# Optimization experiments

Hardware: AMD Instinct MI355X
Metric: run time of the kernel (lower is better)

## Reference

```python
import jax, jax.numpy as jnp
import numpy as np
import math

TOP_K = 10  # top-k codes kept by SOHO_Pre_VD for negative sampling
EPS_LN = 1e-5


def layer_norm(x, w, b):
    mu = jnp.mean(x, axis=-1, keepdims=True)
    var = jnp.mean((x - mu) ** 2, axis=-1, keepdims=True)
    return (x - mu) * jax.lax.rsqrt(var + EPS_LN) * w + b


def position_encoding_sine(b, l, d):
    # mask is all-ones [b, l]; identical across batch, compute once and broadcast
    h = w = int(math.sqrt(l))
    ones = jnp.ones((h, w), jnp.float32)
    y_embed = jnp.cumsum(ones, axis=0)
    x_embed = jnp.cumsum(ones, axis=1)
    eps = 1e-6
    two_pi = 2.0 * np.pi
    y_embed = y_embed / (y_embed[-1:, :] + eps) * two_pi
    x_embed = x_embed / (x_embed[:, -1:] + eps) * two_pi
    pf = d // 2
    dim_t = jnp.arange(pf, dtype=jnp.float32)
    dim_t = 10000.0 ** (2.0 * jnp.floor(dim_t / 2.0) / pf)
    px = x_embed[:, :, None] / dim_t  # [h, w, pf]
    py = y_embed[:, :, None] / dim_t
    # interleave sin(even), cos(odd)
    px = jnp.stack([jnp.sin(px[..., 0::2]), jnp.cos(px[..., 1::2])], axis=-1).reshape(h, w, pf)
    py = jnp.stack([jnp.sin(py[..., 0::2]), jnp.cos(py[..., 1::2])], axis=-1).reshape(h, w, pf)
    pos = jnp.concatenate([py, px], axis=-1).reshape(l, d)  # [l, d]
    return jnp.broadcast_to(pos, (b, l, d))


def setup_inputs() -> dict:
    key = jax.random.key(0)
    ks = jax.random.split(key, 10)
    B, L, CIN, D, K = 16, 576, 1024, 768, 8192
    s = 0.02
    return {
        "img": jax.random.normal(ks[0], (B, L, CIN), jnp.float32),
        "mask_indices": jax.random.randint(ks[1], (B, 1), 0, L),
        "lin_w": jax.random.normal(ks[2], (D, CIN), jnp.float32) * s,
        "lin_b": jnp.zeros((D,), jnp.float32),
        "ln1_w": jnp.ones((D,), jnp.float32),
        "ln1_b": jnp.zeros((D,), jnp.float32),
        "embed": jax.random.normal(ks[3], (K, D), jnp.float32),
        "pos_w": jax.random.normal(ks[4], (D, D), jnp.float32) * s,
        "pos_b": jnp.zeros((D,), jnp.float32),
        "gate_w": jax.random.normal(ks[5], (2, 2 * D), jnp.float32) * s,
        "gate_b": jnp.zeros((2,), jnp.float32),
        "gate_ln_w": jnp.ones((2,), jnp.float32),
        "gate_ln_b": jnp.zeros((2,), jnp.float32),
        "out_ln_w": jnp.ones((D,), jnp.float32),
        "out_ln_b": jnp.zeros((D,), jnp.float32),
    }


def reference(img, mask_indices, lin_w, lin_b, ln1_w, ln1_b, embed, pos_w, pos_b,
              gate_w, gate_b, gate_ln_w, gate_ln_b, out_ln_w, out_ln_b):
    b, l, _ = img.shape
    d = lin_w.shape[0]
    # self.linear: Linear -> LayerNorm -> ReLU
    xq = jax.nn.relu(layer_norm(img @ lin_w.T + lin_b, ln1_w, ln1_b))  # [b,l,d]
    x = xq.reshape(b * l, d)
    # SOHO VQ: nearest code by L2, straight-through
    d2 = (x * x).sum(-1, keepdims=True) - 2.0 * (x @ embed.T) + (embed * embed).sum(-1)  # [N,K]
    idx = jnp.argmin(d2, axis=-1)  # [N]
    quant = jnp.take(embed, idx, axis=0)
    quantized = x + jax.lax.stop_gradient(quant - x)
    probs = jax.nn.softmax(-d2, axis=-1)
    topk_values, topk_indices = jax.lax.top_k(probs, TOP_K)  # [N,K'],[N,K']
    # pos_align linear
    quantized = quantized @ pos_w.T + pos_b
    emb_pt = quantized.reshape(b, l, d)
    # gated fusion
    g = jnp.concatenate([emb_pt, xq], axis=-1) @ gate_w.T + gate_b  # [b,l,2]
    g = jax.nn.relu(layer_norm(g, gate_ln_w, gate_ln_b))
    score = jax.nn.softmax(g, axis=-1)
    emb_s, img_s = score[..., 0:1], score[..., 1:2]
    emb_pt = emb_pt * emb_s + xq * img_s
    pos = position_encoding_sine(b, l, d)
    # negative index construction (visual_mask is all ones)
    ind = idx.reshape(b, l).astype(jnp.float32)  # [b,l]
    masked_labels = jnp.take_along_axis(ind, mask_indices, axis=1)  # [b,1]
    masked_neg = (ind == masked_labels).astype(jnp.float32)[..., None]  # [b,l,1]
    samp = jax.random.categorical(jax.random.key(42), jnp.log(topk_values))  # [N]
    neg = jnp.take_along_axis(topk_indices, samp[:, None], axis=1).reshape(b, l, 1).astype(jnp.float32)
    neg_at_mask = jnp.take_along_axis(neg[..., 0], mask_indices, axis=1)[..., None]  # [b,1,1]
    neg_idx = neg_at_mask * masked_neg + ind[..., None] * (1.0 - masked_neg)  # [b,l,1]
    neg_idx = neg_idx.reshape(b * l).astype(jnp.int32)
    # one-hot matmul == embedding gather
    neg_q = jnp.take(embed, neg_idx, axis=0).reshape(b, l, d)
    neg_q = neg_q * emb_s + jax.lax.stop_gradient(xq) * img_s
    out_pos = layer_norm(emb_pt + pos, out_ln_w, out_ln_b)
    out_neg = layer_norm(neg_q + pos, out_ln_w, out_ln_b)
    return (out_pos, out_neg)
```

## Files before the change

### kernel.cpp

```cpp
#include <hip/hip_runtime.h>
#include <stdint.h>

#define M_TOT  9216
#define D_     768
#define CIN_   1024
#define KCODE  8192
#define TOPK   10

typedef unsigned short u16;
typedef __bf16 bf16x8 __attribute__((ext_vector_type(8)));
typedef float f32x4 __attribute__((ext_vector_type(4)));


__device__ inline float block_sum(float v, float* red) {
    int t = threadIdx.x;
    red[t] = v;
    __syncthreads();
    #pragma unroll
    for (int s = 128; s > 0; s >>= 1) {
        if (t < s) red[t] += red[t + s];
        __syncthreads();
    }
    float r = red[0];
    __syncthreads();
    return r;
}

__device__ inline unsigned long long umin64(unsigned long long a, unsigned long long b) {
    return (a < b) ? a : b;
}

__device__ inline u16 f2bf(float f) {
    uint32_t u = __float_as_uint(f);
    uint32_t r = (u + 0x7fffu + ((u >> 16) & 1u)) >> 16;
    return (u16)r;
}
__device__ inline float bf2f(u16 h) {
    return __uint_as_float(((uint32_t)h) << 16);
}

__device__ inline unsigned long long shfl_xor_u64(unsigned long long v, int mask) {
    int lo = (int)(uint32_t)v, hi = (int)(uint32_t)(v >> 32);
    lo = __shfl_xor(lo, mask, 64);
    hi = __shfl_xor(hi, mask, 64);
    return ((unsigned long long)(uint32_t)hi << 32) | (uint32_t)lo;
}

#define GLDS(gp, lp) __builtin_amdgcn_global_load_lds( \
    (const __attribute__((address_space(1))) unsigned int*)(gp), \
    (__attribute__((address_space(3))) unsigned int*)(lp), 16, 0, 0)

__global__ __launch_bounds__(256) void k_gemm1_mfma(
    const u16* __restrict__ Ah, const u16* __restrict__ Am, const u16* __restrict__ Al,
    const u16* __restrict__ Bh, const u16* __restrict__ Bm, const u16* __restrict__ Bl,
    const float* __restrict__ bias, float* __restrict__ C)
{
    __shared__ __align__(16) u16 sm[24576];
    const int t = threadIdx.x;
    const int lane = t & 63, wid = t >> 6;
    const int row0 = blockIdx.y * 128, col0 = blockIdx.x * 128;
    const int r16 = lane & 15, kb = lane >> 4;
    const int wr = wid >> 1, wc = wid & 1;
    const int sc = (lane & 3) * 8;
    const int lrow = lane >> 2;

    f32x4 acc[4][4];
    #pragma unroll
    for (int mf = 0; mf < 4; ++mf)
        #pragma unroll
        for (int nf = 0; nf < 4; ++nf)
            acc[mf][nf] = (f32x4){0.f, 0.f, 0.f, 0.f};

    for (int k0 = 0; k0 < CIN_; k0 += 32) {
        __syncthreads();
        #pragma unroll
        for (int i = 0; i < 12; ++i) {
            int mat = i >> 1;
            int c = (i & 1) ? wid + 4 : wid;
            const u16* mp = (mat == 0) ? Ah : (mat == 1) ? Am : (mat == 2) ? Al
                          : (mat == 3) ? Bh : (mat == 4) ? Bm : Bl;
            int rbase = (mat < 3) ? row0 : col0;
            const u16* g = mp + (size_t)(rbase + c * 16 + lrow) * CIN_ + k0 + sc;
            GLDS(g, sm + mat * 4096 + c * 512);
        }
        __syncthreads();

        bf16x8 bh[4], bm[4], bl[4];
        #pragma unroll
        for (int nf = 0; nf < 4; ++nf) {
            int offb = 12288 + (wc * 64 + nf * 16 + r16) * 32 + kb * 8;
            bh[nf] = *(const bf16x8*)(sm + offb);
            bm[nf] = *(const bf16x8*)(sm + offb + 4096);
            bl[nf] = *(const bf16x8*)(sm + offb + 8192);
        }
        #pragma unroll
        for (int mf = 0; mf < 4; ++mf) {
            int offa = (wr * 64 + mf * 16 + r16) * 32 + kb * 8;
            bf16x8 ah = *(const bf16x8*)(sm + offa);
            bf16x8 am = *(const bf16x8*)(sm + offa + 4096);
            bf16x8 al = *(const bf16x8*)(sm + offa + 8192);
            #pragma unroll
            for (int nf = 0; nf < 4; ++nf) {
                acc[mf][nf] = __builtin_amdgcn_mfma_f32_16x16x32_bf16(ah, bh[nf], acc[mf][nf], 0, 0, 0);
                acc[mf][nf] = __builtin_amdgcn_mfma_f32_16x16x32_bf16(ah, bm[nf], acc[mf][nf], 0, 0, 0);
                acc[mf][nf] = __builtin_amdgcn_mfma_f32_16x16x32_bf16(am, bh[nf], acc[mf][nf], 0, 0, 0);
                acc[mf][nf] = __builtin_amdgcn_mfma_f32_16x16x32_bf16(am, bm[nf], acc[mf][nf], 0, 0, 0);
                acc[mf][nf] = __builtin_amdgcn_mfma_f32_16x16x32_bf16(ah, bl[nf], acc[mf][nf], 0, 0, 0);
                acc[mf][nf] = __builtin_amdgcn_mfma_f32_16x16x32_bf16(al, bh[nf], acc[mf][nf], 0, 0, 0);
            }
        }
    }

    #pragma unroll
    for (int mf = 0; mf < 4; ++mf) {
        #pragma unroll
        for (int q = 0; q < 4; ++q) {
            int m = row0 + wr * 64 + mf * 16 + kb * 4 + q;
            #pragma unroll
            for (int nf = 0; nf < 4; ++nf) {
                int n = col0 + wc * 64 + nf * 16 + r16;
                C[(size_t)m * D_ + n] = acc[mf][nf][q] + bias[n];
            }
        }
    }
}

__global__ __launch_bounds__(256) void k_gemm3_mfma(
    const u16* __restrict__ Eh, const u16* __restrict__ El,
    const u16* __restrict__ Ph, const u16* __restrict__ Pl,
    const int* __restrict__ gather,
    const float* __restrict__ bias, float* __restrict__ C)
{
    __shared__ __align__(16) u16 sm[16384];
    const int t = threadIdx.x;
    const int lane = t & 63, wid = t >> 6;
    const int row0 = blockIdx.y * 128, col0 = blockIdx.x * 128;
    const int r16 = lane & 15, kb = lane >> 4;
    const int wr = wid >> 1, wc = wid & 1;
    const int sc = (lane & 3) * 8;
    const int lrow = lane >> 2;

    int gi0 = gather[row0 + wid * 16 + lrow];
    int gi1 = gather[row0 + (wid + 4) * 16 + lrow];

    f32x4 acc[4][4];
    #pragma unroll
    for (int mf = 0; mf < 4; ++mf)
        #pragma unroll
        for (int nf = 0; nf < 4; ++nf)
            acc[mf][nf] = (f32x4){0.f, 0.f, 0.f, 0.f};

    for (int k0 = 0; k0 < D_; k0 += 32) {
        __syncthreads();
        #pragma unroll
        for (int i = 0; i < 8; ++i) {
            int mat = i >> 1;
            int c = (i & 1) ? wid + 4 : wid;
            int grow = (i & 1) ? gi1 : gi0;
            const u16* g;
            if (mat == 0)      g = Eh + (size_t)grow * D_ + k0 + sc;
            else if (mat == 1) g = El + (size_t)grow * D_ + k0 + sc;
            else if (mat == 2) g = Ph + (size_t)(col0 + c * 16 + lrow) * D_ + k0 + sc;
            else               g = Pl + (size_t)(col0 + c * 16 + lrow) * D_ + k0 + sc;
            GLDS(g, sm + mat * 4096 + c * 512);
        }
        __syncthreads();

        bf16x8 bh[4], bl[4];
        #pragma unroll
        for (int nf = 0; nf < 4; ++nf) {
            int offb = 8192 + (wc * 64 + nf * 16 + r16) * 32 + kb * 8;
            bh[nf] = *(const bf16x8*)(sm + offb);
            bl[nf] = *(const bf16x8*)(sm + offb + 4096);
        }
        #pragma unroll
        for (int mf = 0; mf < 4; ++mf) {
            int offa = (wr * 64 + mf * 16 + r16) * 32 + kb * 8;
            bf16x8 ah = *(const bf16x8*)(sm + offa);
            bf16x8 al = *(const bf16x8*)(sm + offa + 4096);
            #pragma unroll
            for (int nf = 0; nf < 4; ++nf) {
                acc[mf][nf] = __builtin_amdgcn_mfma_f32_16x16x32_bf16(ah, bh[nf], acc[mf][nf], 0, 0, 0);
                acc[mf][nf] = __builtin_amdgcn_mfma_f32_16x16x32_bf16(ah, bl[nf], acc[mf][nf], 0, 0, 0);
                acc[mf][nf] = __builtin_amdgcn_mfma_f32_16x16x32_bf16(al, bh[nf], acc[mf][nf], 0, 0, 0);
            }
        }
    }

    #pragma unroll
    for (int mf = 0; mf < 4; ++mf) {
        #pragma unroll
        for (int q = 0; q < 4; ++q) {
            int m = row0 + wr * 64 + mf * 16 + kb * 4 + q;
            #pragma unroll
            for (int nf = 0; nf < 4; ++nf) {
                int n = col0 + wc * 64 + nf * 16 + r16;
                C[(size_t)m * D_ + n] = acc[mf][nf][q] + bias[n];
            }
        }
    }
}

__global__ __launch_bounds__(256) void k_gemm2_mfma(
    const u16* __restrict__ Xh, const u16* __restrict__ Xl,
    const u16* __restrict__ Eh, const u16* __restrict__ El,
    const float* __restrict__ xsq, const float* __restrict__ esq,
    unsigned long long* __restrict__ amin)
{
    __shared__ __align__(16) u16 sm[32768];
    const int t = threadIdx.x;
    const int lane = t & 63, wid = t >> 6;
    const int row0 = blockIdx.y * 128, col0 = blockIdx.x * 128;
    const int r16 = lane & 15, kb = lane >> 4;
    const int wr = wid >> 1, wc = wid & 1;

    f32x4 acc[4][4];
    #pragma unroll
    for (int mf = 0; mf < 4; ++mf)
        #pragma unroll
        for (int nf = 0; nf < 4; ++nf)
            acc[mf][nf] = (f32x4){0.f, 0.f, 0.f, 0.f};

    const u16* sb = (wid == 0) ? Xh : (wid == 1) ? Xl : (wid == 2) ? Eh : El;
    const int rbase = (wid < 2) ? row0 : col0;
    const u16* srcb = sb + (size_t)(rbase + (lane >> 3)) * D_
                         + ((lane & 7) ^ (lane >> 3)) * 8;
    u16* dstb = sm + wid * 8192 + lane * 8;

    const int swz = (r16 & 7);
    for (int kt = 0; kt < 12; ++kt) {
        __syncthreads();
        #pragma unroll
        for (int c = 0; c < 16; ++c) {
            GLDS(srcb + kt * 64 + c * 8 * D_, dstb + c * 512);
        }
        __syncthreads();
        #pragma unroll
        for (int h = 0; h < 2; ++h) {
            const int slot = ((h * 4 + kb) ^ swz) * 8;
            bf16x8 bh[4], bl[4];
            #pragma unroll
            for (int nf = 0; nf < 4; ++nf) {
                int off = (wc * 64 + nf * 16 + r16) * 64 + slot;
                bh[nf] = *(const bf16x8*)(sm + 16384 + off);
                bl[nf] = *(const bf16x8*)(sm + 24576 + off);
            }
            #pragma unroll
            for (int mf = 0; mf < 4; ++mf) {
                int off = (wr * 64 + mf * 16 + r16) * 64 + slot;
                bf16x8 ah = *(const bf16x8*)(sm + off);
                bf16x8 al = *(const bf16x8*)(sm + 8192 + off);
                #pragma unroll
                for (int nf = 0; nf < 4; ++nf) {
                    acc[mf][nf] = __builtin_amdgcn_mfma_f32_16x16x32_bf16(ah, bh[nf], acc[mf][nf], 0, 0, 0);
                    acc[mf][nf] = __builtin_amdgcn_mfma_f32_16x16x32_bf16(ah, bl[nf], acc[mf][nf], 0, 0, 0);
                    acc[mf][nf] = __builtin_amdgcn_mfma_f32_16x16x32_bf16(al, bh[nf], acc[mf][nf], 0, 0, 0);
                }
            }
        }
    }

    float esqv[4];
    #pragma unroll
    for (int nf = 0; nf < 4; ++nf)
        esqv[nf] = esq[col0 + wc * 64 + nf * 16 + r16];

    #pragma unroll
    for (int mf = 0; mf < 4; ++mf) {
        #pragma unroll
        for (int q = 0; q < 4; ++q) {
            int m = row0 + wr * 64 + mf * 16 + kb * 4 + q;
            float xsv = xsq[m];
            unsigned long long best = ~0ull;
            #pragma unroll
            for (int nf = 0; nf < 4; ++nf) {
                int n = col0 + wc * 64 + nf * 16 + r16;
                float d2 = (xsv - 2.0f * acc[mf][nf][q]) + esqv[nf];
                unsigned long long key =
                    ((unsigned long long)__float_as_uint(d2) << 32) | (unsigned)n;
                best = umin64(best, key);
            }
            #pragma unroll
            for (int msk = 1; msk < 16; msk <<= 1)
                best = umin64(best, shfl_xor_u64(best, msk));
            if (r16 == 0) atomicMin(&amin[m], best);
        }
    }
}

__global__ __launch_bounds__(256) void k_split3(const float* __restrict__ in,
    u16* __restrict__ h, u16* __restrict__ m, u16* __restrict__ l, int n4)
{
    int i = blockIdx.x * 256 + threadIdx.x;
    int stride = gridDim.x * 256;
    for (; i < n4; i += stride) {
        float4 v = ((const float4*)in)[i];
        ushort4 hv, mv, lv;
        float x, r;
        x = v.x; hv.x = f2bf(x); r = x - bf2f(hv.x); mv.x = f2bf(r); lv.x = f2bf(r - bf2f(mv.x));
        x = v.y; hv.y = f2bf(x); r = x - bf2f(hv.y); mv.y = f2bf(r); lv.y = f2bf(r - bf2f(mv.y));
        x = v.z; hv.z = f2bf(x); r = x - bf2f(hv.z); mv.z = f2bf(r); lv.z = f2bf(r - bf2f(mv.z));
        x = v.w; hv.w = f2bf(x); r = x - bf2f(hv.w); mv.w = f2bf(r); lv.w = f2bf(r - bf2f(mv.w));
        ((ushort4*)h)[i] = hv; ((ushort4*)m)[i] = mv; ((ushort4*)l)[i] = lv;
    }
}

__global__ __launch_bounds__(256) void k_split2(const float* __restrict__ in,
    u16* __restrict__ h, u16* __restrict__ l, int n4)
{
    int i = blockIdx.x * 256 + threadIdx.x;
    int stride = gridDim.x * 256;
    for (; i < n4; i += stride) {
        float4 v = ((const float4*)in)[i];
        ushort4 hv, lv;
        hv.x = f2bf(v.x); lv.x = f2bf(v.x - bf2f(hv.x));
        hv.y = f2bf(v.y); lv.y = f2bf(v.y - bf2f(hv.y));
        hv.z = f2bf(v.z); lv.z = f2bf(v.z - bf2f(hv.z));
        hv.w = f2bf(v.w); lv.w = f2bf(v.w - bf2f(hv.w));
        ((ushort4*)h)[i] = hv; ((ushort4*)l)[i] = lv;
    }
}

__global__ __launch_bounds__(256) void k_ln_relu(
    const float* __restrict__ in, const float* __restrict__ w,
    const float* __restrict__ b, float* __restrict__ xq, float* __restrict__ xsq,
    u16* __restrict__ Xh, u16* __restrict__ Xl)
{
    __shared__ float red[256];
    int r = blockIdx.x, t = threadIdx.x;
    const float* row = in + (size_t)r * D_;
    float v0 = row[t], v1 = row[t + 256], v2 = row[t + 512];
    float mu = block_sum(v0 + v1 + v2, red) * (1.0f / 768.0f);
    float d0 = v0 - mu, d1 = v1 - mu, d2 = v2 - mu;
    float var = block_sum(d0 * d0 + d1 * d1 + d2 * d2, red) * (1.0f / 768.0f);
    float rn = 1.0f / sqrtf(var + 1e-5f);
    float o0 = fmaxf(0.0f, d0 * rn * w[t] + b[t]);
    float o1 = fmaxf(0.0f, d1 * rn * w[t + 256] + b[t + 256]);
    float o2 = fmaxf(0.0f, d2 * rn * w[t + 512] + b[t + 512]);
    float* orow = xq + (size_t)r * D_;
    orow[t] = o0; orow[t + 256] = o1; orow[t + 512] = o2;
    u16 h0 = f2bf(o0), h1 = f2bf(o1), h2 = f2bf(o2);
    Xh[(size_t)r * D_ + t]       = h0;
    Xh[(size_t)r * D_ + t + 256] = h1;
    Xh[(size_t)r * D_ + t + 512] = h2;
    Xl[(size_t)r * D_ + t]       = f2bf(o0 - bf2f(h0));
    Xl[(size_t)r * D_ + t + 256] = f2bf(o1 - bf2f(h1));
    Xl[(size_t)r * D_ + t + 512] = f2bf(o2 - bf2f(h2));
    float q = block_sum(o0 * o0 + o1 * o1 + o2 * o2, red);
    if (t == 0) xsq[r] = q;
}

__global__ __launch_bounds__(256) void k_esq(const float* __restrict__ E,
                                             float* __restrict__ esq,
                                             u16* __restrict__ Eh,
                                             u16* __restrict__ El)
{
    __shared__ float red[256];
    int r = blockIdx.x, t = threadIdx.x;
    const float* row = E + (size_t)r * D_;
    float v0 = row[t], v1 = row[t + 256], v2 = row[t + 512];
    u16 h0 = f2bf(v0), h1 = f2bf(v1), h2 = f2bf(v2);
    Eh[(size_t)r * D_ + t]       = h0;
    Eh[(size_t)r * D_ + t + 256] = h1;
    Eh[(size_t)r * D_ + t + 512] = h2;
    El[(size_t)r * D_ + t]       = f2bf(v0 - bf2f(h0));
    El[(size_t)r * D_ + t + 256] = f2bf(v1 - bf2f(h1));
    El[(size_t)r * D_ + t + 512] = f2bf(v2 - bf2f(h2));
    float s = block_sum(v0 * v0 + v1 * v1 + v2 * v2, red);
    if (t == 0) esq[r] = s;
}

__global__ void k_extract(const unsigned long long* __restrict__ amin,
                          int* __restrict__ idx, int n)
{
    int i = blockIdx.x * 256 + threadIdx.x;
    if (i < n) idx[i] = (int)(amin[i] & 0xFFFFFFFFull);
}

__global__ __launch_bounds__(256) void k_gate(
    const float* __restrict__ embpt, const float* __restrict__ xq,
    const float* __restrict__ gw, const float* __restrict__ gb,
    const float* __restrict__ glnw, const float* __restrict__ glnb,
    float* __restrict__ scores)
{
    __shared__ float red[256];
    int r = blockIdx.x, t = threadIdx.x;
    const float* ep = embpt + (size_t)r * D_;
    const float* xr = xq + (size_t)r * D_;
    float g0 = 0.0f, g1 = 0.0f;
    for (int k = t; k < 1536; k += 256) {
        float v = (k < 768) ? ep[k] : xr[k - 768];
        g0 = fmaf(v, gw[k], g0);
        g1 = fmaf(v, gw[1536 + k], g1);
    }
    g0 = block_sum(g0, red);
    g1 = block_sum(g1, red);
    if (t == 0) {
        g0 += gb[0]; g1 += gb[1];
        float mu = 0.5f * (g0 + g1);
        float h0 = g0 - mu, h1 = g1 - mu;
        float var = 0.5f * (h0 * h0 + h1 * h1);
        float rn = 1.0f / sqrtf(var + 1e-5f);
        float o0 = fmaxf(0.0f, h0 * rn * glnw[0] + glnb[0]);
        float o1 = fmaxf(0.0f, h1 * rn * glnw[1] + glnb[1]);
        float m = fmaxf(o0, o1);
        float e0 = expf(o0 - m), e1 = expf(o1 - m);
        float inv = 1.0f / (e0 + e1);
        scores[r * 2 + 0] = e0 * inv;
        scores[r * 2 + 1] = e1 * inv;
    }
}

__global__ __launch_bounds__(256) void k_pos(float* __restrict__ pos)
{
    int l = blockIdx.x, t = threadIdx.x;
    for (int k = t; k < D_; k += 256) {
        int kk = (k < 384) ? k : k - 384;
        int m = kk >> 1;
        float coord = (k < 384) ? (float)(l / 24) : (float)(l % 24);
        float v = (coord + 1.0f) / 24.000001f * 6.28318530717958647692f;
        float tm = exp2f((float)m * (13.287712379549449f / 192.0f));
        float a = v / tm;
        pos[(size_t)l * D_ + k] = (kk & 1) ? cosf(a) : sinf(a);
    }
}

__global__ __launch_bounds__(256) void k_d2row(
    const float* __restrict__ xq, const float* __restrict__ E,
    const float* __restrict__ xsq, const float* __restrict__ esq,
    const int* __restrict__ mask, float* __restrict__ d2row)
{
    __shared__ float xs[768];
    int b = blockIdx.x;
    int g = blockIdx.y;
    int t = threadIdx.x;
    int r = b * 576 + mask[b];
    xs[t]       = xq[(size_t)r * D_ + t];
    xs[t + 256] = xq[(size_t)r * D_ + t + 256];
    xs[t + 512] = xq[(size_t)r * D_ + t + 512];
    __syncthreads();
    int lane = t & 63, w = t >> 6;
    float xsr = xsq[r];
    for (int e = 0; e < 16; ++e) {
        int j = g * 64 + w * 16 + e;
        const float* er = E + (size_t)j * D_;
        float p = 0.0f;
        for (int k = lane; k < D_; k += 64) p = fmaf(xs[k], er[k], p);
        #pragma unroll
        for (int off = 32; off > 0; off >>= 1) p += __shfl_down(p, off);
        if (lane == 0) d2row[b * KCODE + j] = (xsr - 2.0f * p) + esq[j];
    }
}

__device__ inline void threefry2x32(uint32_t x0, uint32_t x1,
                                    uint32_t& o0, uint32_t& o1)
{
    const uint32_t ks0 = 0u, ks1 = 42u;
    const uint32_t ks2 = ks0 ^ ks1 ^ 0x1BD11BDAu;
    uint32_t ks[3] = {ks0, ks1, ks2};
    x0 += ks[0]; x1 += ks[1];
    const int R0[4] = {13, 15, 26, 6};
    const int R1[4] = {17, 29, 16, 24};
    #pragma unroll
    for (int i = 0; i < 5; ++i) {
        const int* R = (i & 1) ? R1 : R0;
        #pragma unroll
        for (int q = 0; q < 4; ++q) {
            x0 += x1;
            x1 = (x1 << R[q]) | (x1 >> (32 - R[q]));
            x1 ^= x0;
        }
        x0 += ks[(i + 1) % 3];
        x1 += ks[(i + 2) % 3] + (uint32_t)(i + 1);
    }
    o0 = x0; o1 = x1;
}

__global__ __launch_bounds__(256) void k_topk_sample(
    const float* __restrict__ d2row, const unsigned long long* __restrict__ amin,
    const int* __restrict__ mask, int* __restrict__ mlabel, int* __restrict__ negsel)
{
    __shared__ float sd2[KCODE];
    __shared__ unsigned long long rbuf[256];
    __shared__ float rfs[256];
    __shared__ int sel[TOPK];
    __shared__ float selv[TOPK];
    __shared__ float sS;
    int b = blockIdx.x, t = threadIdx.x;
    for (int j = t; j < KCODE; j += 256) sd2[j] = d2row[b * KCODE + j];
    __syncthreads();
    for (int p = 0; p < TOPK; ++p) {
        unsigned long long best = ~0ull;
        for (int j = t; j < KCODE; j += 256) {
            bool skip = false;
            for (int q = 0; q < p; ++q) skip = skip || (j == sel[q]);
            if (skip) continue;
            unsigned long long key =
                ((unsigned long long)__float_as_uint(sd2[j]) << 32) | (unsigned)j;
            best = umin64(best, key);
        }
        rbuf[t] = best;
        __syncthreads();
        for (int s = 128; s > 0; s >>= 1) {
            if (t < s) rbuf[t] = umin64(rbuf[t], rbuf[t + s]);
            __syncthreads();
        }
        if (t == 0) {
            sel[p] = (int)(rbuf[0] & 0xFFFFFFFFull);
            selv[p] = __uint_as_float((uint32_t)(rbuf[0] >> 32));
        }
        __syncthreads();
    }
    float d2min = selv[0];
    float part = 0.0f;
    for (int j = t; j < KCODE; j += 256) part += expf(d2min - sd2[j]);
    part = block_sum(part, rfs);
    if (t == 0) sS = part;
    __syncthreads();
    if (t == 0) {
        int rb = b * 576 + mask[b];
        mlabel[b] = (int)(amin[rb] & 0xFFFFFFFFull);
        float S = sS;
        float bestv = 0.0f;
        int samp = 0;
        bool first = true;
        for (int k = 0; k < TOPK; ++k) {
            float pk = expf(d2min - selv[k]) / S;
            float logit = logf(pk);
            unsigned f = (unsigned)(rb * 10 + k);
            uint32_t o0, o1;
            threefry2x32(0u, f, o0, o1);
            uint32_t bits = o0 ^ o1;
            float uu = __uint_as_float(0x3F800000u | (bits >> 9)) - 1.0f;
            uu = uu + 1.1754944e-38f;
            uu = fmaxf(1.1754944e-38f, uu);
            float gum = -logf(-logf(uu));
            float sc = logit + gum;
            if (first || sc > bestv) { bestv = sc; samp = k; first = false; }
        }
        negsel[b] = sel[samp];
    }
}

__global__ __launch_bounds__(256) void k_final(
    const float* __restrict__ embpt, const float* __restrict__ xq,
    const float* __restrict__ scores, const int* __restrict__ idx,
    const int* __restrict__ mlabel, const int* __restrict__ negsel,
    const float* __restrict__ E, const float* __restrict__ pos,
    const float* __restrict__ ow, const float* __restrict__ ob,
    float* __restrict__ outp, float* __restrict__ outn)
{
    __shared__ float red[256];
    int r = blockIdx.x, t = threadIdx.x;
    int b = r / 576, l = r % 576;
    float s0 = scores[r * 2 + 0], s1 = scores[r * 2 + 1];
    int ir = idx[r];
    int nidx = (ir == mlabel[b]) ? negsel[b] : ir;
    const float* ep = embpt + (size_t)r * D_;
    const float* xr = xq + (size_t)r * D_;
    const float* er = E + (size_t)nidx * D_;
    const float* pr = pos + (size_t)l * D_;
    float vp[3], vn[3];
    #pragma unroll
    for (int q = 0; q < 3; ++q) {
        int k = t + q * 256;
        float xv = xr[k] * s1;
        float pv = pr[k];
        vp[q] = (ep[k] * s0 + xv) + pv;
        vn[q] = (er[k] * s0 + xv) + pv;
    }
    float mup = block_sum(vp[0] + vp[1] + vp[2], red) * (1.0f / 768.0f);
    float a0 = vp[0] - mup, a1 = vp[1] - mup, a2 = vp[2] - mup;
    float varp = block_sum(a0 * a0 + a1 * a1 + a2 * a2, red) * (1.0f / 768.0f);
    float rnp = 1.0f / sqrtf(varp + 1e-5f);
    float mun = block_sum(vn[0] + vn[1] + vn[2], red) * (1.0f / 768.0f);
    float c0 = vn[0] - mun, c1 = vn[1] - mun, c2 = vn[2] - mun;
    float varn = block_sum(c0 * c0 + c1 * c1 + c2 * c2, red) * (1.0f / 768.0f);
    float rnn = 1.0f / sqrtf(varn + 1e-5f);
    float* op = outp + (size_t)r * D_;
    float* on = outn + (size_t)r * D_;
    op[t]       = a0 * rnp * ow[t]       + ob[t];
    op[t + 256] = a1 * rnp * ow[t + 256] + ob[t + 256];
    op[t + 512] = a2 * rnp * ow[t + 512] + ob[t + 512];
    on[t]       = c0 * rnn * ow[t]       + ob[t];
    on[t + 256] = c1 * rnn * ow[t + 256] + ob[t + 256];
    on[t + 512] = c2 * rnn * ow[t + 512] + ob[t + 512];
}

extern "C" void kernel_launch(void* const* d_in, const int* in_sizes, int n_in,
                              void* d_out, int out_size, void* d_ws, size_t ws_size,
                              hipStream_t stream)
{
    (void)in_sizes; (void)n_in; (void)out_size; (void)ws_size;
    const float* img    = (const float*)d_in[0];
    const int*   maski  = (const int*)d_in[1];
    const float* lin_w  = (const float*)d_in[2];
    const float* lin_b  = (const float*)d_in[3];
    const float* ln1_w  = (const float*)d_in[4];
    const float* ln1_b  = (const float*)d_in[5];
    const float* embed  = (const float*)d_in[6];
    const float* pos_w  = (const float*)d_in[7];
    const float* pos_b  = (const float*)d_in[8];
    const float* gate_w = (const float*)d_in[9];
    const float* gate_b = (const float*)d_in[10];
    const float* glnw   = (const float*)d_in[11];
    const float* glnb   = (const float*)d_in[12];
    const float* olnw   = (const float*)d_in[13];
    const float* olnb   = (const float*)d_in[14];

    uint8_t* wp = (uint8_t*)d_ws;
    auto alloc = [&](size_t bytes) -> void* {
        void* p = (void*)wp;
        wp += (bytes + 255) & ~(size_t)255;
        return p;
    };
    float* bufA = (float*)alloc((size_t)M_TOT * D_ * 4);
    float* xq   = (float*)alloc((size_t)M_TOT * D_ * 4);
    float* xsq  = (float*)alloc((size_t)M_TOT * 4);
    float* esq  = (float*)alloc((size_t)KCODE * 4);
    unsigned long long* amin = (unsigned long long*)alloc((size_t)M_TOT * 8);
    int*   idxA   = (int*)alloc((size_t)M_TOT * 4);
    float* scores = (float*)alloc((size_t)M_TOT * 2 * 4);
    float* posb   = (float*)alloc((size_t)576 * D_ * 4);
    float* d2row  = (float*)alloc((size_t)16 * KCODE * 4);
    int*   mlab   = (int*)alloc(16 * 4);
    int*   negsel = (int*)alloc(16 * 4);
    u16* Wh = (u16*)alloc((size_t)D_ * CIN_ * 2);
    u16* Wm = (u16*)alloc((size_t)D_ * CIN_ * 2);
    u16* Wl = (u16*)alloc((size_t)D_ * CIN_ * 2);
    u16* Ph = (u16*)alloc((size_t)D_ * D_ * 2);
    u16* Pl = (u16*)alloc((size_t)D_ * D_ * 2);
    u16* R  = (u16*)alloc((size_t)3 * M_TOT * CIN_ * 2);
    u16* Ih = R;
    u16* Im = R + (size_t)M_TOT * CIN_;
    u16* Il = R + (size_t)2 * M_TOT * CIN_;
    u16* Xh = R;
    u16* Xl = Xh + (size_t)M_TOT * D_;
    u16* Eh = Xl + (size_t)M_TOT * D_;
    u16* El = Eh + (size_t)KCODE * D_;

    float* outp = (float*)d_out;
    float* outn = outp + (size_t)M_TOT * D_;

    hipMemsetAsync(amin, 0xFF, M_TOT * sizeof(unsigned long long), stream);

    dim3 blk(256);
    k_split3<<<2048, blk, 0, stream>>>(img, Ih, Im, Il, M_TOT * CIN_ / 4);
    k_split3<<<768, blk, 0, stream>>>(lin_w, Wh, Wm, Wl, D_ * CIN_ / 4);
    k_split2<<<576, blk, 0, stream>>>(pos_w, Ph, Pl, D_ * D_ / 4);
    k_gemm1_mfma<<<dim3(D_ / 128, M_TOT / 128), blk, 0, stream>>>(
        Ih, Im, Il, Wh, Wm, Wl, lin_b, bufA);
    k_ln_relu<<<M_TOT, blk, 0, stream>>>(bufA, ln1_w, ln1_b, xq, xsq, Xh, Xl);
    k_esq<<<KCODE, blk, 0, stream>>>(embed, esq, Eh, El);
    k_gemm2_mfma<<<dim3(KCODE / 128, M_TOT / 128), blk, 0, stream>>>(
        Xh, Xl, Eh, El, xsq, esq, amin);
    k_extract<<<M_TOT / 256, blk, 0, stream>>>(amin, idxA, M_TOT);
    k_gemm3_mfma<<<dim3(D_ / 128, M_TOT / 128), blk, 0, stream>>>(
        Eh, El, Ph, Pl, idxA, pos_b, bufA);
    k_gate<<<M_TOT, blk, 0, stream>>>(bufA, xq, gate_w, gate_b, glnw, glnb, scores);
    k_pos<<<576, blk, 0, stream>>>(posb);
    k_d2row<<<dim3(16, KCODE / 64), blk, 0, stream>>>(xq, embed, xsq, esq, maski, d2row);
    k_topk_sample<<<16, blk, 0, stream>>>(d2row, amin, maski, mlab, negsel);
    k_final<<<M_TOT, blk, 0, stream>>>(bufA, xq, scores, idxA, mlab, negsel,
                                       embed, posb, olnw, olnb, outp, outn);
}
```

Before: 818.7 us.

## Double-buffer gemm2 LDS loads and fold masked-row distance output into it

The distance GEMM now double-buffers its shared-memory tiles, prefetching the next K slice while MFMAs run on the current one, and batches the MFMA issue by term. It also writes the full distance row for each batch's masked row directly from the epilogue, using a precomputed row-flag array. This removes the separate fp32 k_d2row kernel that re-read the whole codebook. Shared memory doubles to 128KB per block, which may lower occupancy. The d2row values now come from the split-bf16 path rather than full fp32, so they can differ slightly from before.

```diff
diff --git a/kernel.cpp b/kernel.cpp
--- a/kernel.cpp
+++ b/kernel.cpp
@@ -201,13 +201,23 @@
     }
 }
 
+__global__ void k_rowflag(const int* __restrict__ mask, int* __restrict__ rowflag)
+{
+    int i = blockIdx.x * 256 + threadIdx.x;
+    if (i < M_TOT) {
+        int b = i / 576, l = i - b * 576;
+        rowflag[i] = (mask[b] == l) ? (b + 1) : 0;
+    }
+}
+
 __global__ __launch_bounds__(256) void k_gemm2_mfma(
     const u16* __restrict__ Xh, const u16* __restrict__ Xl,
     const u16* __restrict__ Eh, const u16* __restrict__ El,
     const float* __restrict__ xsq, const float* __restrict__ esq,
+    const int* __restrict__ rowflag, float* __restrict__ d2row,
     unsigned long long* __restrict__ amin)
 {
-    __shared__ __align__(16) u16 sm[32768];
+    __shared__ __align__(16) u16 sm[2][32768];
     const int t = threadIdx.x;
     const int lane = t & 63, wid = t >> 6;
     const int row0 = blockIdx.y * 128, col0 = blockIdx.x * 128;
@@ -225,39 +235,54 @@
     const int rbase = (wid < 2) ? row0 : col0;
     const u16* srcb = sb + (size_t)(rbase + (lane >> 3)) * D_
                          + ((lane & 7) ^ (lane >> 3)) * 8;
-    u16* dstb = sm + wid * 8192 + lane * 8;
+
+    for (int c = 0; c < 16; ++c)
+        GLDS(srcb + c * 8 * D_, sm[0] + wid * 8192 + lane * 8 + c * 512);
+    __syncthreads();
 
     const int swz = (r16 & 7);
     for (int kt = 0; kt < 12; ++kt) {
-        __syncthreads();
-        #pragma unroll
-        for (int c = 0; c < 16; ++c) {
-            GLDS(srcb + kt * 64 + c * 8 * D_, dstb + c * 512);
-        }
-        __syncthreads();
+        int cur = kt & 1;
+        if (kt < 11) {
+            u16* dstb = sm[cur ^ 1] + wid * 8192 + lane * 8;
+            #pragma unroll
+            for (int c = 0; c < 16; ++c)
+                GLDS(srcb + (kt + 1) * 64 + c * 8 * D_, dstb + c * 512);
+        }
+        const u16* B = sm[cur];
         #pragma unroll
         for (int h = 0; h < 2; ++h) {
             const int slot = ((h * 4 + kb) ^ swz) * 8;
-            bf16x8 bh[4], bl[4];
+            bf16x8 ah[4], al[4], bh[4], bl[4];
             #pragma unroll
             for (int nf = 0; nf < 4; ++nf) {
                 int off = (wc * 64 + nf * 16 + r16) * 64 + slot;
-                bh[nf] = *(const bf16x8*)(sm + 16384 + off);
-                bl[nf] = *(const bf16x8*)(sm + 24576 + off);
+                bh[nf] = *(const bf16x8*)(B + 16384 + off);
+                bl[nf] = *(const bf16x8*)(B + 24576 + off);
             }
             #pragma unroll
             for (int mf = 0; mf < 4; ++mf) {
                 int off = (wr * 64 + mf * 16 + r16) * 64 + slot;
-                bf16x8 ah = *(const bf16x8*)(sm + off);
-                bf16x8 al = *(const bf16x8*)(sm + 8192 + off);
+                ah[mf] = *(const bf16x8*)(B + off);
+                al[mf] = *(const bf16x8*)(B + 8192 + off);
+            }
+            #pragma unroll
+            for (int mf = 0; mf < 4; ++mf)
                 #pragma unroll
-                for (int nf = 0; nf < 4; ++nf) {
-                    acc[mf][nf] = __builtin_amdgcn_mfma_f32_16x16x32_bf16(ah, bh[nf], acc[mf][nf], 0, 0, 0);
-                    acc[mf][nf] = __builtin_amdgcn_mfma_f32_16x16x32_bf16(ah, bl[nf], acc[mf][nf], 0, 0, 0);
-                    acc[mf][nf] = __builtin_amdgcn_mfma_f32_16x16x32_bf16(al, bh[nf], acc[mf][nf], 0, 0, 0);
-                }
-            }
-        }
+                for (int nf = 0; nf < 4; ++nf)
+                    acc[mf][nf] = __builtin_amdgcn_mfma_f32_16x16x32_bf16(ah[mf], bh[nf], acc[mf][nf], 0, 0, 0);
+            #pragma unroll
+            for (int mf = 0; mf < 4; ++mf)
+                #pragma unroll
+                for (int nf = 0; nf < 4; ++nf)
+                    acc[mf][nf] = __builtin_amdgcn_mfma_f32_16x16x32_bf16(ah[mf], bl[nf], acc[mf][nf], 0, 0, 0);
+            #pragma unroll
+            for (int mf = 0; mf < 4; ++mf)
+                #pragma unroll
+                for (int nf = 0; nf < 4; ++nf)
+                    acc[mf][nf] = __builtin_amdgcn_mfma_f32_16x16x32_bf16(al[mf], bh[nf], acc[mf][nf], 0, 0, 0);
+        }
+        __syncthreads();
     }
 
     float esqv[4];
@@ -271,11 +296,13 @@
         for (int q = 0; q < 4; ++q) {
             int m = row0 + wr * 64 + mf * 16 + kb * 4 + q;
             float xsv = xsq[m];
+            int rf = rowflag[m];
             unsigned long long best = ~0ull;
             #pragma unroll
             for (int nf = 0; nf < 4; ++nf) {
                 int n = col0 + wc * 64 + nf * 16 + r16;
                 float d2 = (xsv - 2.0f * acc[mf][nf][q]) + esqv[nf];
+                if (rf) d2row[(size_t)(rf - 1) * KCODE + n] = d2;
                 unsigned long long key =
                     ((unsigned long long)__float_as_uint(d2) << 32) | (unsigned)n;
                 best = umin64(best, key);
@@ -422,33 +449,6 @@
         float tm = exp2f((float)m * (13.287712379549449f / 192.0f));
         float a = v / tm;
         pos[(size_t)l * D_ + k] = (kk & 1) ? cosf(a) : sinf(a);
-    }
-}
-
-__global__ __launch_bounds__(256) void k_d2row(
-    const float* __restrict__ xq, const float* __restrict__ E,
-    const float* __restrict__ xsq, const float* __restrict__ esq,
-    const int* __restrict__ mask, float* __restrict__ d2row)
-{
-    __shared__ float xs[768];
-    int b = blockIdx.x;
-    int g = blockIdx.y;
-    int t = threadIdx.x;
-    int r = b * 576 + mask[b];
-    xs[t]       = xq[(size_t)r * D_ + t];
-    xs[t + 256] = xq[(size_t)r * D_ + t + 256];
-    xs[t + 512] = xq[(size_t)r * D_ + t + 512];
-    __syncthreads();
-    int lane = t & 63, w = t >> 6;
-    float xsr = xsq[r];
-    for (int e = 0; e < 16; ++e) {
-        int j = g * 64 + w * 16 + e;
-        const float* er = E + (size_t)j * D_;
-        float p = 0.0f;
-        for (int k = lane; k < D_; k += 64) p = fmaf(xs[k], er[k], p);
-        #pragma unroll
-        for (int off = 32; off > 0; off >>= 1) p += __shfl_down(p, off);
-        if (lane == 0) d2row[b * KCODE + j] = (xsr - 2.0f * p) + esq[j];
     }
 }
 
@@ -620,6 +620,7 @@
     float* esq  = (float*)alloc((size_t)KCODE * 4);
     unsigned long long* amin = (unsigned long long*)alloc((size_t)M_TOT * 8);
     int*   idxA   = (int*)alloc((size_t)M_TOT * 4);
+    int*   rowflag = (int*)alloc((size_t)M_TOT * 4);
     float* scores = (float*)alloc((size_t)M_TOT * 2 * 4);
     float* posb   = (float*)alloc((size_t)576 * D_ * 4);
     float* d2row  = (float*)alloc((size_t)16 * KCODE * 4);
@@ -648,18 +649,18 @@
     k_split3<<<2048, blk, 0, stream>>>(img, Ih, Im, Il, M_TOT * CIN_ / 4);
     k_split3<<<768, blk, 0, stream>>>(lin_w, Wh, Wm, Wl, D_ * CIN_ / 4);
     k_split2<<<576, blk, 0, stream>>>(pos_w, Ph, Pl, D_ * D_ / 4);
+    k_rowflag<<<M_TOT / 256, blk, 0, stream>>>(maski, rowflag);
     k_gemm1_mfma<<<dim3(D_ / 128, M_TOT / 128), blk, 0, stream>>>(
         Ih, Im, Il, Wh, Wm, Wl, lin_b, bufA);
     k_ln_relu<<<M_TOT, blk, 0, stream>>>(bufA, ln1_w, ln1_b, xq, xsq, Xh, Xl);
     k_esq<<<KCODE, blk, 0, stream>>>(embed, esq, Eh, El);
     k_gemm2_mfma<<<dim3(KCODE / 128, M_TOT / 128), blk, 0, stream>>>(
-        Xh, Xl, Eh, El, xsq, esq, amin);
+        Xh, Xl, Eh, El, xsq, esq, rowflag, d2row, amin);
     k_extract<<<M_TOT / 256, blk, 0, stream>>>(amin, idxA, M_TOT);
     k_gemm3_mfma<<<dim3(D_ / 128, M_TOT / 128), blk, 0, stream>>>(
         Eh, El, Ph, Pl, idxA, pos_b, bufA);
     k_gate<<<M_TOT, blk, 0, stream>>>(bufA, xq, gate_w, gate_b, glnw, glnb, scores);
     k_pos<<<576, blk, 0, stream>>>(posb);
-    k_d2row<<<dim3(16, KCODE / 64), blk, 0, stream>>>(xq, embed, xsq, esq, maski, d2row);
     k_topk_sample<<<16, blk, 0, stream>>>(d2row, amin, maski, mlab, negsel);
     k_final<<<M_TOT, blk, 0, stream>>>(bufA, xq, scores, idxA, mlab, negsel,
                                        embed, posb, olnw, olnb, outp, outn);
```

Measured after the change: 935.3 us. +14.2%, slower.
